# Performance work log

Measured on AMD Instinct MI355X. Metric: run time of the kernel, lower is better.

Reference implementation:

```python
import jax, jax.numpy as jnp
import numpy as np

B_SZ, SEQ, D_MODEL, D_INNER, D_STATE, D_CONV = 2, 2048, 768, 1536, 16, 4
EPS = 1e-6


def setup_inputs() -> dict:
    key = jax.random.key(0)
    ks = jax.random.split(key, 8)
    sc = lambda n: 1.0 / np.sqrt(n)
    x = jax.random.normal(ks[0], (B_SZ, SEQ, D_MODEL), jnp.float32)
    norm_w = jnp.ones((D_MODEL,), jnp.float32)
    w_in = jax.random.normal(ks[1], (D_MODEL, 2 * D_INNER), jnp.float32) * sc(D_MODEL)
    conv_w = jax.random.normal(ks[2], (D_INNER, D_CONV), jnp.float32) * sc(D_CONV)
    conv_b = jnp.zeros((D_INNER,), jnp.float32)
    w_x = jax.random.normal(ks[3], (D_INNER, 2 * D_STATE + 1), jnp.float32) * sc(D_INNER)
    w_dt = jax.random.normal(ks[4], (D_INNER,), jnp.float32)
    b_dt = jnp.zeros((D_INNER,), jnp.float32)
    A_log = jnp.log(jnp.broadcast_to(jnp.arange(1, D_STATE + 1, dtype=jnp.float32), (D_INNER, D_STATE)))
    D = jnp.ones((D_INNER,), jnp.float32)
    w_out = jax.random.normal(ks[5], (D_INNER, D_MODEL), jnp.float32) * sc(D_INNER)
    return dict(x=x, norm_w=norm_w, w_in=w_in, conv_w=conv_w, conv_b=conv_b,
                w_x=w_x, w_dt=w_dt, b_dt=b_dt, A_log=A_log, D=D, w_out=w_out)


def _rmsnorm(x, w):
    xf = x.astype(jnp.float32)
    rms = jax.lax.rsqrt(jnp.mean(xf * xf, axis=-1, keepdims=True) + EPS)
    return (xf * rms).astype(x.dtype) * w


def _silu(x):
    return x * jax.nn.sigmoid(x)


def _s6_forward(x, norm_w, w_in, conv_w, conv_b, w_x, w_dt, b_dt, A_log, D, w_out):
    Bsz, S, Dm = x.shape
    Di, K = conv_w.shape
    Ds = A_log.shape[1]
    residual = x
    xn = _rmsnorm(x, norm_w)
    xz = xn @ w_in                                 # (B,S,2*Di)
    x_main, z = jnp.split(xz, 2, axis=-1)
    # causal depthwise conv1d: pad left K-1, keep first S outputs
    lhs = x_main.transpose(0, 2, 1)                # (B,Di,S)
    rhs = conv_w[:, None, :]                       # (Di,1,K)
    conv = jax.lax.conv_general_dilated(
        lhs, rhs, window_strides=(1,), padding=[(K - 1, 0)],
        dimension_numbers=('NCH', 'OIH', 'NCH'), feature_group_count=Di)
    x_main = (conv + conv_b[None, :, None]).transpose(0, 2, 1)  # (B,S,Di)
    x_main = _silu(x_main)
    x_ssm = x_main @ w_x                           # (B,S,2*Ds+1)
    Bp = x_ssm[..., :Ds]                           # (B,S,Ds)
    Cp = x_ssm[..., Ds:2 * Ds]                     # (B,S,Ds)
    dt_raw = x_ssm[..., -1:]                       # (B,S,1)
    dt = jax.nn.softplus(dt_raw * w_dt[None, None, :] + b_dt)  # (B,S,Di)
    A = -jnp.exp(A_log)                            # (Di,Ds)

    def step(h, inp):
        xt, dtt, Bt, Ct = inp                      # (B,Di),(B,Di),(B,Ds),(B,Ds)
        dA = jnp.exp(A[None] * dtt[..., None])     # (B,Di,Ds)
        h = dA * h + (dtt * xt)[..., None] * Bt[:, None, :]
        y = jnp.einsum('bds,bs->bd', h, Ct)
        return h, y

    h0 = jnp.zeros((Bsz, Di, Ds), x_main.dtype)
    xs = (x_main.transpose(1, 0, 2), dt.transpose(1, 0, 2),
          Bp.transpose(1, 0, 2), Cp.transpose(1, 0, 2))
    _, ys = jax.lax.scan(step, h0, xs)             # ys: (S,B,Di)
    y = ys.transpose(1, 0, 2)
    y = y + x_main * D
    y = y * _silu(z)
    return residual + y @ w_out                    # dropout is identity at eval


def reference(x, norm_w, w_in, conv_w, conv_b, w_x, w_dt, b_dt, A_log, D, w_out):
    return _s6_forward(x, norm_w, w_in, conv_w, conv_b, w_x, w_dt, b_dt, A_log, D, w_out)
```

## Files before the change

### kernel.cpp

```cpp
#include <hip/hip_runtime.h>
#include <math.h>


#define DM   768
#define DI   1536
#define DS2  16
#define SEQN 2048
#define BSZ  2
#define NROWS (BSZ*SEQN)
#define CHUNK 32
#define NCHUNK (SEQN/CHUNK)

#define AS1 __attribute__((address_space(1)))
#define AS3 __attribute__((address_space(3)))

typedef short short8 __attribute__((ext_vector_type(8)));
typedef short short4v __attribute__((ext_vector_type(4)));
typedef float f32x4 __attribute__((ext_vector_type(4)));

__device__ __forceinline__ unsigned short f2bf(float f) {
  unsigned u = __builtin_bit_cast(unsigned, f);
  unsigned r = (u + 0x7FFFu + ((u >> 16) & 1u)) >> 16;
  return (unsigned short)r;
}
__device__ __forceinline__ float bf2f(short s) {
  unsigned u = ((unsigned)(unsigned short)s) << 16;
  return __builtin_bit_cast(float, u);
}

template<int N> __device__ __forceinline__ void waitcnt_vm() {
  if constexpr (N == 0)      asm volatile("s_waitcnt vmcnt(0)" ::: "memory");
  else if constexpr (N == 2) asm volatile("s_waitcnt vmcnt(2)" ::: "memory");
  else if constexpr (N == 3) asm volatile("s_waitcnt vmcnt(3)" ::: "memory");
  else if constexpr (N == 4) asm volatile("s_waitcnt vmcnt(4)" ::: "memory");
  else if constexpr (N == 6) asm volatile("s_waitcnt vmcnt(6)" ::: "memory");
}

__device__ __forceinline__ void transpose_body(const float* __restrict__ src,
                                               int rows, int cols,
                                               short* __restrict__ dst,
                                               int bx, int by, int tid) {
  __shared__ float t[32][33];
  int r0 = by * 32, c0 = bx * 32;
  int lr = tid >> 3, lc4 = (tid & 7) * 4;
  float4 v = *reinterpret_cast<const float4*>(&src[(size_t)(r0 + lr) * cols + c0 + lc4]);
  t[lr][lc4 + 0] = v.x; t[lr][lc4 + 1] = v.y; t[lr][lc4 + 2] = v.z; t[lr][lc4 + 3] = v.w;
  __syncthreads();
  int orow = tid >> 3, oc4 = (tid & 7) * 4;
  short4v o;
  o.x = (short)f2bf(t[oc4 + 0][orow]); o.y = (short)f2bf(t[oc4 + 1][orow]);
  o.z = (short)f2bf(t[oc4 + 2][orow]); o.w = (short)f2bf(t[oc4 + 3][orow]);
  *reinterpret_cast<short4v*>(&dst[(size_t)(c0 + orow) * rows + r0 + oc4]) = o;
}

__global__ __launch_bounds__(256) void prep_k(
    const float* __restrict__ x, const float* __restrict__ nw,
    short* __restrict__ xn,
    const float* __restrict__ w_in, short* __restrict__ winT,
    const float* __restrict__ w_out, short* __restrict__ woutT,
    const float* __restrict__ wx, short* __restrict__ wxT48) {
  const int bid = blockIdx.x;
  const int tid = threadIdx.x;
  if (bid < 1024) {
    int wv = tid >> 6, lane = tid & 63;
    int row = bid * 4 + wv;
    const float* xr = x + (size_t)row * DM;
    float4 v[3];
    float s = 0.f;
#pragma unroll
    for (int i = 0; i < 3; ++i) {
      v[i] = *reinterpret_cast<const float4*>(&xr[(i * 64 + lane) * 4]);
      s = fmaf(v[i].x, v[i].x, s); s = fmaf(v[i].y, v[i].y, s);
      s = fmaf(v[i].z, v[i].z, s); s = fmaf(v[i].w, v[i].w, s);
    }
#pragma unroll
    for (int off = 32; off >= 1; off >>= 1) s += __shfl_xor(s, off, 64);
    float rs = rsqrtf(s * (1.f / DM) + 1e-6f);
#pragma unroll
    for (int i = 0; i < 3; ++i) {
      const float4 w = *reinterpret_cast<const float4*>(&nw[(i * 64 + lane) * 4]);
      short4v o;
      o.x = (short)f2bf(v[i].x * rs * w.x); o.y = (short)f2bf(v[i].y * rs * w.y);
      o.z = (short)f2bf(v[i].z * rs * w.z); o.w = (short)f2bf(v[i].w * rs * w.w);
      *reinterpret_cast<short4v*>(&xn[(size_t)row * DM + (i * 64 + lane) * 4]) = o;
    }
  } else if (bid < 1024 + 2304) {
    int i2 = bid - 1024;
    transpose_body(w_in, DM, 2 * DI, winT, i2 % 96, i2 / 96, tid);
  } else if (bid < 1024 + 2304 + 1152) {
    int i3 = bid - (1024 + 2304);
    transpose_body(w_out, DI, DM, woutT, i3 % 24, i3 / 24, tid);
  } else {
    int idx = (bid - (1024 + 2304 + 1152)) * 256 + tid;
    if (idx < DI * 33) {
      int k = idx / 33, j = idx % 33;
      wxT48[(size_t)j * DI + k] = (short)f2bf(wx[idx]);
    }
  }
}

template<int BM, int BN, bool OUTBF>
__global__ __launch_bounds__(512) void gemm_bf16(
    const short* __restrict__ A, int lda,
    const short* __restrict__ Bt, int ldb,
    void* __restrict__ Cv, int ldc, int K,
    const float* __restrict__ res, int ldr)
{
  constexpr int WM = BM / 2, WN = BN / 4;
  constexpr int MI = WM / 16, NJ = WN / 16;
  constexpr int ACH = BM / 8, BCH = BN / 8;
  constexpr int CPW = (ACH + BCH) / 8;
  static_assert((ACH + BCH) % 8 == 0, "chunks must split across 8 waves");
  __shared__ __align__(16) short As[2 * BM * 64];
  __shared__ __align__(16) short Bs[2 * BN * 64];
  const int tid = threadIdx.x;
  const int w = tid >> 6, lane = tid & 63;
  const int wr = w >> 2, wc = w & 3;
  const int m0 = blockIdx.y * BM, n0 = blockIdx.x * BN;
  const int l15 = lane & 15, l4 = lane >> 4;
  const int srow = lane >> 3;
  const int ksw = (((lane & 7) ^ srow) * 8);
  const int rx = l15 & 7;

  f32x4 acc[MI][NJ];
#pragma unroll
  for (int i = 0; i < MI; ++i)
#pragma unroll
    for (int j = 0; j < NJ; ++j) acc[i][j] = (f32x4){0.f, 0.f, 0.f, 0.f};

  auto STAGE = [&](int buf, int k0) {
#pragma unroll
    for (int q = 0; q < CPW; ++q) {
      int c = w * CPW + q;
      if (c < ACH) {
        __builtin_amdgcn_global_load_lds(
            (const AS1 unsigned int*)(A + (size_t)(m0 + 8 * c + srow) * lda + k0 + ksw),
            (AS3 unsigned int*)((char*)As + buf * (BM * 128) + c * 1024), 16, 0, 0);
      } else {
        int c2 = c - ACH;
        __builtin_amdgcn_global_load_lds(
            (const AS1 unsigned int*)(Bt + (size_t)(n0 + 8 * c2 + srow) * ldb + k0 + ksw),
            (AS3 unsigned int*)((char*)Bs + buf * (BN * 128) + c2 * 1024), 16, 0, 0);
      }
    }
  };

  STAGE(0, 0);
  int cur = 0;
  const int NT = K / 64;
  for (int t = 0; t < NT; ++t) {
    __builtin_amdgcn_sched_barrier(0);
    __builtin_amdgcn_s_barrier();
    if (t + 1 < NT) {
      STAGE(cur ^ 1, (t + 1) * 64);
      waitcnt_vm<CPW>();
    } else {
      waitcnt_vm<0>();
    }
    __builtin_amdgcn_sched_barrier(0);
    __builtin_amdgcn_s_barrier();
    __builtin_amdgcn_sched_barrier(0);
    const short* Ab = As + cur * BM * 64;
    const short* Bb = Bs + cur * BN * 64;
    __builtin_amdgcn_s_setprio(1);
#pragma unroll
    for (int kk = 0; kk < 2; ++kk) {
      short8 a[MI], b[NJ];
#pragma unroll
      for (int i = 0; i < MI; ++i)
        a[i] = *reinterpret_cast<const short8*>(
            &Ab[(wr * WM + i * 16 + l15) * 64 + (((kk * 4 + l4) ^ rx) * 8)]);
#pragma unroll
      for (int j = 0; j < NJ; ++j)
        b[j] = *reinterpret_cast<const short8*>(
            &Bb[(wc * WN + j * 16 + l15) * 64 + (((kk * 4 + l4) ^ rx) * 8)]);
#pragma unroll
      for (int i = 0; i < MI; ++i)
#pragma unroll
        for (int j = 0; j < NJ; ++j)
          acc[i][j] = __builtin_amdgcn_mfma_f32_16x16x32_bf16(a[i], b[j], acc[i][j], 0, 0, 0);
    }
    __builtin_amdgcn_s_setprio(0);
    cur ^= 1;
  }

#pragma unroll
  for (int i = 0; i < MI; ++i) {
#pragma unroll
    for (int j = 0; j < NJ; ++j) {
      int col = n0 + wc * WN + j * 16 + l15;
#pragma unroll
      for (int r = 0; r < 4; ++r) {
        int row = m0 + wr * WM + i * 16 + l4 * 4 + r;
        float v = acc[i][j][r];
        if constexpr (OUTBF) {
          ((short*)Cv)[(size_t)row * ldc + col] = (short)f2bf(v);
        } else {
          if (res) v += res[(size_t)row * ldr + col];
          ((float*)Cv)[(size_t)row * ldc + col] = v;
        }
      }
    }
  }
}

__global__ __launch_bounds__(256) void conv_silu_k(const short* __restrict__ xz,
                                                   const float* __restrict__ cw,
                                                   const float* __restrict__ cb,
                                                   short* __restrict__ xc) {
  int idx = blockIdx.x * 256 + threadIdx.x;
  int d8 = (idx % (DI / 8)) * 8;
  int bt = idx / (DI / 8);
  int t = bt & (SEQN - 1);
  short8 rb[4];
#pragma unroll
  for (int rr = 0; rr < 4; ++rr) {
    int trow = t - 3 + rr;
    rb[rr] = (trow >= 0)
        ? *reinterpret_cast<const short8*>(&xz[(size_t)(bt - 3 + rr) * 3072 + d8])
        : (short8){0, 0, 0, 0, 0, 0, 0, 0};
  }
  const float4 ba = *reinterpret_cast<const float4*>(&cb[d8]);
  const float4 bbq = *reinterpret_cast<const float4*>(&cb[d8 + 4]);
  const float bias[8] = {ba.x, ba.y, ba.z, ba.w, bbq.x, bbq.y, bbq.z, bbq.w};
  short8 o;
#pragma unroll
  for (int i = 0; i < 8; ++i) {
    const float4 cwv = *reinterpret_cast<const float4*>(&cw[(size_t)(d8 + i) * 4]);
    float acc = bias[i];
    acc = fmaf(bf2f(rb[0][i]), cwv.x, acc);
    acc = fmaf(bf2f(rb[1][i]), cwv.y, acc);
    acc = fmaf(bf2f(rb[2][i]), cwv.z, acc);
    acc = fmaf(bf2f(rb[3][i]), cwv.w, acc);
    o[i] = (short)f2bf(acc / (1.f + __expf(-acc)));
  }
  *reinterpret_cast<short8*>(&xc[(size_t)bt * DI + d8]) = o;
}

__global__ __launch_bounds__(512) void xssm_gemm_k(
    const short* __restrict__ xc, const short* __restrict__ wxT48,
    float* __restrict__ xout)
{
  __shared__ float red[8][16][48];
  const int tid = threadIdx.x;
  const int wv = tid >> 6, lane = tid & 63;
  const int l15 = lane & 15, l4 = lane >> 4;
  const int m0 = blockIdx.x * 16;
  const int kbase = wv * 192 + l4 * 8;

  f32x4 acc[3];
#pragma unroll
  for (int j = 0; j < 3; ++j) acc[j] = (f32x4){0.f, 0.f, 0.f, 0.f};

  const short* arow = xc + (size_t)(m0 + l15) * DI + kbase;
#pragma unroll
  for (int ks = 0; ks < 6; ++ks) {
    short8 a = *reinterpret_cast<const short8*>(arow + ks * 32);
#pragma unroll
    for (int j = 0; j < 3; ++j) {
      short8 b = *reinterpret_cast<const short8*>(
          &wxT48[(size_t)(j * 16 + l15) * DI + kbase + ks * 32]);
      acc[j] = __builtin_amdgcn_mfma_f32_16x16x32_bf16(a, b, acc[j], 0, 0, 0);
    }
  }
#pragma unroll
  for (int j = 0; j < 3; ++j)
#pragma unroll
    for (int r = 0; r < 4; ++r)
      red[wv][l4 * 4 + r][j * 16 + l15] = acc[j][r];
  __syncthreads();
  for (int i = tid; i < 16 * 48; i += 512) {
    int row = i / 48, col = i % 48;
    float s = 0.f;
#pragma unroll
    for (int v = 0; v < 8; ++v) s += red[v][row][col];
    xout[(size_t)(m0 + row) * 48 + col] = s;
  }
}

__global__ __launch_bounds__(256) void scan_part1(
    const short* __restrict__ xc,
    const float* __restrict__ xout,
    const float* __restrict__ w_dt, const float* __restrict__ b_dt,
    const float* __restrict__ A_log,
    float* __restrict__ hL, float* __restrict__ Tsum)
{
  const int blk = blockIdx.x;
  const int c  = blk % NCHUNK;
  const int db = (blk / NCHUNK) % (DI / 256);
  const int b  = blk / (NCHUNK * (DI / 256));
  const int tid = threadIdx.x;
  const int d = db * 256 + tid;
  const size_t cb = (size_t)b * SEQN + c * CHUNK;

  __shared__ float sB[CHUNK][16];
  __shared__ float sdt[CHUNK];
  if (tid < CHUNK * 4) {
    int row = tid >> 2, q = tid & 3;
    *reinterpret_cast<float4*>(&sB[row][q * 4]) =
        *reinterpret_cast<const float4*>(&xout[(cb + row) * 48 + q * 4]);
  }
  if (tid < CHUNK) sdt[tid] = xout[(cb + tid) * 48 + 32];
  __syncthreads();

  const float wdt = w_dt[d], bdt = b_dt[d];
  float a[DS2], h[DS2];
#pragma unroll
  for (int q = 0; q < 4; ++q) {
    float4 al = *reinterpret_cast<const float4*>(&A_log[(size_t)d * DS2 + q * 4]);
    a[q * 4 + 0] = -__expf(al.x); a[q * 4 + 1] = -__expf(al.y);
    a[q * 4 + 2] = -__expf(al.z); a[q * 4 + 3] = -__expf(al.w);
  }
#pragma unroll
  for (int n = 0; n < DS2; ++n) h[n] = 0.f;
  float T = 0.f;

#pragma unroll 2
  for (int tt = 0; tt < CHUNK; ++tt) {
    float v = fmaf(sdt[tt], wdt, bdt);
    float dtv = (v > 15.f) ? v : __logf(1.f + __expf(v));
    T += dtv;
    float xv = bf2f(xc[(cb + tt) * DI + d]);
    float s = dtv * xv;
    float bb[DS2];
#pragma unroll
    for (int q = 0; q < 4; ++q)
      *reinterpret_cast<float4*>(&bb[q * 4]) =
          *reinterpret_cast<const float4*>(&sB[tt][q * 4]);
#pragma unroll
    for (int n = 0; n < DS2; ++n)
      h[n] = fmaf(__expf(a[n] * dtv), h[n], s * bb[n]);
  }

  const size_t base = (size_t)(b * NCHUNK + c) * DI + d;
#pragma unroll
  for (int q = 0; q < 4; ++q)
    *reinterpret_cast<float4*>(&hL[base * 16 + q * 4]) =
        *reinterpret_cast<const float4*>(&h[q * 4]);
  Tsum[base] = T;
}

__global__ __launch_bounds__(256) void scan_combine_k(
    float* __restrict__ hLH, const float* __restrict__ Tsum,
    const float* __restrict__ A_log)
{
  int g = blockIdx.x * 256 + threadIdx.x;
  int n = g & 15;
  int d = (g >> 4) % DI;
  int b = g / (DI * DS2);
  const float a = -__expf(A_log[(size_t)d * DS2 + n]);
  float h = 0.f;
  for (int c = 0; c < NCHUNK; ++c) {
    size_t base = (size_t)(b * NCHUNK + c) * DI + d;
    float hl = hLH[base * 16 + n];
    float T = Tsum[base];
    float hprev = h;
    h = fmaf(__expf(a * T), h, hl);
    hLH[base * 16 + n] = hprev;
  }
}

__global__ __launch_bounds__(256) void scan_part3(
    const short* __restrict__ xc,
    const short* __restrict__ xz,
    short* __restrict__ ybf,
    const float* __restrict__ xout,
    const float* __restrict__ w_dt, const float* __restrict__ b_dt,
    const float* __restrict__ A_log, const float* __restrict__ Dp,
    const float* __restrict__ Hinit)
{
  const int blk = blockIdx.x;
  const int c  = blk % NCHUNK;
  const int db = (blk / NCHUNK) % (DI / 256);
  const int b  = blk / (NCHUNK * (DI / 256));
  const int tid = threadIdx.x;
  const int d = db * 256 + tid;
  const size_t cb = (size_t)b * SEQN + c * CHUNK;

  __shared__ float sB[CHUNK][16], sC[CHUNK][16];
  __shared__ float sdt[CHUNK];
  if (tid < CHUNK * 4) {
    int row = tid >> 2, q = tid & 3;
    *reinterpret_cast<float4*>(&sB[row][q * 4]) =
        *reinterpret_cast<const float4*>(&xout[(cb + row) * 48 + q * 4]);
  } else if (tid < CHUNK * 8) {
    int i = tid - CHUNK * 4;
    int row = i >> 2, q = i & 3;
    *reinterpret_cast<float4*>(&sC[row][q * 4]) =
        *reinterpret_cast<const float4*>(&xout[(cb + row) * 48 + 16 + q * 4]);
  }
  if (tid < CHUNK) sdt[tid] = xout[(cb + tid) * 48 + 32];

  const float wdt = w_dt[d], bdt = b_dt[d];
  const float Dd = Dp[d];
  float a[DS2], h[DS2];
#pragma unroll
  for (int q = 0; q < 4; ++q) {
    float4 al = *reinterpret_cast<const float4*>(&A_log[(size_t)d * DS2 + q * 4]);
    a[q * 4 + 0] = -__expf(al.x); a[q * 4 + 1] = -__expf(al.y);
    a[q * 4 + 2] = -__expf(al.z); a[q * 4 + 3] = -__expf(al.w);
  }
  const size_t base = (size_t)(b * NCHUNK + c) * DI + d;
#pragma unroll
  for (int q = 0; q < 4; ++q)
    *reinterpret_cast<float4*>(&h[q * 4]) =
        *reinterpret_cast<const float4*>(&Hinit[base * 16 + q * 4]);
  __syncthreads();

#pragma unroll 2
  for (int tt = 0; tt < CHUNK; ++tt) {
    float v = fmaf(sdt[tt], wdt, bdt);
    float dtv = (v > 15.f) ? v : __logf(1.f + __expf(v));
    float xv = bf2f(xc[(cb + tt) * DI + d]);
    float s = dtv * xv;
    float bb[DS2], cc[DS2];
#pragma unroll
    for (int q = 0; q < 4; ++q) {
      *reinterpret_cast<float4*>(&bb[q * 4]) =
          *reinterpret_cast<const float4*>(&sB[tt][q * 4]);
      *reinterpret_cast<float4*>(&cc[q * 4]) =
          *reinterpret_cast<const float4*>(&sC[tt][q * 4]);
    }
    float y = 0.f;
#pragma unroll
    for (int n = 0; n < DS2; ++n) {
      h[n] = fmaf(__expf(a[n] * dtv), h[n], s * bb[n]);
      y = fmaf(h[n], cc[n], y);
    }
    const size_t rr = cb + tt;
    float z = bf2f(xz[rr * 3072 + DI + d]);
    float yo = fmaf(xv, Dd, y);
    ybf[rr * DI + d] = (short)f2bf(yo * (z / (1.f + __expf(-z))));
  }
}

extern "C" void kernel_launch(void* const* d_in, const int* in_sizes, int n_in,
                              void* d_out, int out_size, void* d_ws, size_t ws_size,
                              hipStream_t stream) {
  const float* x      = (const float*)d_in[0];
  const float* norm_w = (const float*)d_in[1];
  const float* w_in   = (const float*)d_in[2];
  const float* conv_w = (const float*)d_in[3];
  const float* conv_b = (const float*)d_in[4];
  const float* w_x    = (const float*)d_in[5];
  const float* w_dt   = (const float*)d_in[6];
  const float* b_dt   = (const float*)d_in[7];
  const float* A_log  = (const float*)d_in[8];
  const float* Dp     = (const float*)d_in[9];
  const float* w_out  = (const float*)d_in[10];
  float* out = (float*)d_out;

  float* ws   = (float*)d_ws;
  float* xout = ws;
  float* hL   = xout + (size_t)NROWS * 48;
  float* Tsum = hL + (size_t)BSZ * NCHUNK * DI * 16;
  short* wxT48= (short*)(Tsum + (size_t)BSZ * NCHUNK * DI);
  short* xzb  = wxT48 + (size_t)48 * DI;
  short* xcb  = xzb + (size_t)NROWS * 2 * DI;
  short* xnb  = xcb + (size_t)NROWS * DI;
  short* winT = xnb + (size_t)NROWS * DM;
  short* woutT= winT + (size_t)2 * DI * DM;
  short* ybf  = woutT + (size_t)DM * DI;

  prep_k<<<1024 + 2304 + 1152 + 198, 256, 0, stream>>>(
      x, norm_w, xnb, w_in, winT, w_out, woutT, w_x, wxT48);

  gemm_bf16<128, 128, true><<<dim3(2 * DI / 128, NROWS / 128), 512, 0, stream>>>(
      xnb, DM, winT, DM, xzb, 2 * DI, DM, nullptr, 0);

  conv_silu_k<<<(NROWS * DI / 8) / 256, 256, 0, stream>>>(xzb, conv_w, conv_b, xcb);
  xssm_gemm_k<<<NROWS / 16, 512, 0, stream>>>(xcb, wxT48, xout);

  const int nblk = BSZ * (DI / 256) * NCHUNK;
  scan_part1<<<nblk, 256, 0, stream>>>(xcb, xout, w_dt, b_dt, A_log, hL, Tsum);
  scan_combine_k<<<(BSZ * DI * DS2) / 256, 256, 0, stream>>>(hL, Tsum, A_log);
  scan_part3<<<nblk, 256, 0, stream>>>(xcb, xzb, ybf, xout, w_dt, b_dt,
                                       A_log, Dp, hL);

  gemm_bf16<128, 64, false><<<dim3(DM / 64, NROWS / 128), 512, 0, stream>>>(
      ybf, DI, woutT, DI, out, DM, DI, x, DM);
}
```

Before: 154.6 us.

## Fuse conv+SiLU into x-projection GEMM and remap GEMM blocks for XCD locality

Merges the causal depthwise conv + SiLU kernel into the small x_ssm projection GEMM. Each block computes its 16 rows of conv output into LDS and still writes them to global memory for the scan kernels. This removes one launch and the global re-read of xc. The bf16 GEMM gains a configurable wave grid, with the output GEMM switched to a 4x2 wave layout, and a block-id remap that groups consecutive tiles onto the same XCD (chiplet) for L2 reuse. The fused kernel uses about 49KB of LDS per block, which may lower occupancy.

```diff
diff --git a/kernel.cpp b/kernel.cpp
--- a/kernel.cpp
+++ b/kernel.cpp
@@ -30,10 +30,8 @@
 
 template<int N> __device__ __forceinline__ void waitcnt_vm() {
   if constexpr (N == 0)      asm volatile("s_waitcnt vmcnt(0)" ::: "memory");
-  else if constexpr (N == 2) asm volatile("s_waitcnt vmcnt(2)" ::: "memory");
   else if constexpr (N == 3) asm volatile("s_waitcnt vmcnt(3)" ::: "memory");
   else if constexpr (N == 4) asm volatile("s_waitcnt vmcnt(4)" ::: "memory");
-  else if constexpr (N == 6) asm volatile("s_waitcnt vmcnt(6)" ::: "memory");
 }
 
 __device__ __forceinline__ void transpose_body(const float* __restrict__ src,
@@ -99,24 +97,29 @@
   }
 }
 
-template<int BM, int BN, bool OUTBF>
+template<int BM, int BN, int WGM, int WGN, bool OUTBF>
 __global__ __launch_bounds__(512) void gemm_bf16(
     const short* __restrict__ A, int lda,
     const short* __restrict__ Bt, int ldb,
     void* __restrict__ Cv, int ldc, int K,
     const float* __restrict__ res, int ldr)
 {
-  constexpr int WM = BM / 2, WN = BN / 4;
+  constexpr int WM = BM / WGM, WN = BN / WGN;
   constexpr int MI = WM / 16, NJ = WN / 16;
   constexpr int ACH = BM / 8, BCH = BN / 8;
   constexpr int CPW = (ACH + BCH) / 8;
-  static_assert((ACH + BCH) % 8 == 0, "chunks must split across 8 waves");
+  static_assert(WGM * WGN == 8 && (ACH + BCH) % 8 == 0, "wave/chunk split");
   __shared__ __align__(16) short As[2 * BM * 64];
   __shared__ __align__(16) short Bs[2 * BN * 64];
   const int tid = threadIdx.x;
   const int w = tid >> 6, lane = tid & 63;
-  const int wr = w >> 2, wc = w & 3;
-  const int m0 = blockIdx.y * BM, n0 = blockIdx.x * BN;
+  const int wr = w / WGN, wc = w % WGN;
+
+  const int nwg = gridDim.x * gridDim.y;
+  const int lid = blockIdx.y * gridDim.x + blockIdx.x;
+  const int orig = (lid & 7) * (nwg >> 3) + (lid >> 3);
+  const int m0 = (orig / gridDim.x) * BM, n0 = (orig % gridDim.x) * BN;
+
   const int l15 = lane & 15, l4 = lane >> 4;
   const int srow = lane >> 3;
   const int ksw = (((lane & 7) ^ srow) * 8);
@@ -204,58 +207,62 @@
   }
 }
 
-__global__ __launch_bounds__(256) void conv_silu_k(const short* __restrict__ xz,
-                                                   const float* __restrict__ cw,
-                                                   const float* __restrict__ cb,
-                                                   short* __restrict__ xc) {
-  int idx = blockIdx.x * 256 + threadIdx.x;
-  int d8 = (idx % (DI / 8)) * 8;
-  int bt = idx / (DI / 8);
-  int t = bt & (SEQN - 1);
-  short8 rb[4];
-#pragma unroll
-  for (int rr = 0; rr < 4; ++rr) {
-    int trow = t - 3 + rr;
-    rb[rr] = (trow >= 0)
-        ? *reinterpret_cast<const short8*>(&xz[(size_t)(bt - 3 + rr) * 3072 + d8])
-        : (short8){0, 0, 0, 0, 0, 0, 0, 0};
-  }
-  const float4 ba = *reinterpret_cast<const float4*>(&cb[d8]);
-  const float4 bbq = *reinterpret_cast<const float4*>(&cb[d8 + 4]);
-  const float bias[8] = {ba.x, ba.y, ba.z, ba.w, bbq.x, bbq.y, bbq.z, bbq.w};
-  short8 o;
-#pragma unroll
-  for (int i = 0; i < 8; ++i) {
-    const float4 cwv = *reinterpret_cast<const float4*>(&cw[(size_t)(d8 + i) * 4]);
-    float acc = bias[i];
-    acc = fmaf(bf2f(rb[0][i]), cwv.x, acc);
-    acc = fmaf(bf2f(rb[1][i]), cwv.y, acc);
-    acc = fmaf(bf2f(rb[2][i]), cwv.z, acc);
-    acc = fmaf(bf2f(rb[3][i]), cwv.w, acc);
-    o[i] = (short)f2bf(acc / (1.f + __expf(-acc)));
-  }
-  *reinterpret_cast<short8*>(&xc[(size_t)bt * DI + d8]) = o;
-}
-
-__global__ __launch_bounds__(512) void xssm_gemm_k(
-    const short* __restrict__ xc, const short* __restrict__ wxT48,
-    float* __restrict__ xout)
+__global__ __launch_bounds__(512) void xssm_fused_k(
+    const short* __restrict__ xz,
+    const float* __restrict__ cw, const float* __restrict__ cb,
+    const short* __restrict__ wxT48,
+    short* __restrict__ xc, float* __restrict__ xout)
 {
+  constexpr int LP = 1544;
+  __shared__ __align__(16) short xs[16 * LP];
   __shared__ float red[8][16][48];
   const int tid = threadIdx.x;
+  const int m0 = blockIdx.x * 16;
+
+#pragma unroll
+  for (int i = 0; i < 6; ++i) {
+    const int task = i * 512 + tid;
+    const int row = task / 192;
+    const int g8 = (task % 192) * 8;
+    const int bt = m0 + row;
+    const int t = bt & (SEQN - 1);
+    short8 rb[4];
+#pragma unroll
+    for (int rr = 0; rr < 4; ++rr) {
+      int trow = t - 3 + rr;
+      rb[rr] = (trow >= 0)
+          ? *reinterpret_cast<const short8*>(&xz[(size_t)(bt - 3 + rr) * 3072 + g8])
+          : (short8){0, 0, 0, 0, 0, 0, 0, 0};
+    }
+    const float4 ba = *reinterpret_cast<const float4*>(&cb[g8]);
+    const float4 bbq = *reinterpret_cast<const float4*>(&cb[g8 + 4]);
+    const float bias[8] = {ba.x, ba.y, ba.z, ba.w, bbq.x, bbq.y, bbq.z, bbq.w};
+    short8 o;
+#pragma unroll
+    for (int ii = 0; ii < 8; ++ii) {
+      const float4 cwv = *reinterpret_cast<const float4*>(&cw[(size_t)(g8 + ii) * 4]);
+      float acc = bias[ii];
+      acc = fmaf(bf2f(rb[0][ii]), cwv.x, acc);
+      acc = fmaf(bf2f(rb[1][ii]), cwv.y, acc);
+      acc = fmaf(bf2f(rb[2][ii]), cwv.z, acc);
+      acc = fmaf(bf2f(rb[3][ii]), cwv.w, acc);
+      o[ii] = (short)f2bf(acc / (1.f + __expf(-acc)));
+    }
+    *reinterpret_cast<short8*>(&xc[(size_t)bt * DI + g8]) = o;
+    *reinterpret_cast<short8*>(&xs[row * LP + g8]) = o;
+  }
+  __syncthreads();
+
   const int wv = tid >> 6, lane = tid & 63;
   const int l15 = lane & 15, l4 = lane >> 4;
-  const int m0 = blockIdx.x * 16;
   const int kbase = wv * 192 + l4 * 8;
 
   f32x4 acc[3];
 #pragma unroll
   for (int j = 0; j < 3; ++j) acc[j] = (f32x4){0.f, 0.f, 0.f, 0.f};
-
-  const short* arow = xc + (size_t)(m0 + l15) * DI + kbase;
 #pragma unroll
   for (int ks = 0; ks < 6; ++ks) {
-    short8 a = *reinterpret_cast<const short8*>(arow + ks * 32);
+    short8 a = *reinterpret_cast<const short8*>(&xs[l15 * LP + kbase + ks * 32]);
 #pragma unroll
     for (int j = 0; j < 3; ++j) {
       short8 b = *reinterpret_cast<const short8*>(
@@ -465,11 +472,11 @@
   prep_k<<<1024 + 2304 + 1152 + 198, 256, 0, stream>>>(
       x, norm_w, xnb, w_in, winT, w_out, woutT, w_x, wxT48);
 
-  gemm_bf16<128, 128, true><<<dim3(2 * DI / 128, NROWS / 128), 512, 0, stream>>>(
+  gemm_bf16<128, 128, 2, 4, true><<<dim3(2 * DI / 128, NROWS / 128), 512, 0, stream>>>(
       xnb, DM, winT, DM, xzb, 2 * DI, DM, nullptr, 0);
 
-  conv_silu_k<<<(NROWS * DI / 8) / 256, 256, 0, stream>>>(xzb, conv_w, conv_b, xcb);
-  xssm_gemm_k<<<NROWS / 16, 512, 0, stream>>>(xcb, wxT48, xout);
+  xssm_fused_k<<<NROWS / 16, 512, 0, stream>>>(xzb, conv_w, conv_b, wxT48,
+                                               xcb, xout);
 
   const int nblk = BSZ * (DI / 256) * NCHUNK;
   scan_part1<<<nblk, 256, 0, stream>>>(xcb, xout, w_dt, b_dt, A_log, hL, Tsum);
@@ -477,6 +484,6 @@
   scan_part3<<<nblk, 256, 0, stream>>>(xcb, xzb, ybf, xout, w_dt, b_dt,
                                        A_log, Dp, hL);
 
-  gemm_bf16<128, 64, false><<<dim3(DM / 64, NROWS / 128), 512, 0, stream>>>(
+  gemm_bf16<128, 64, 4, 2, false><<<dim3(DM / 64, NROWS / 128), 512, 0, stream>>>(
       ybf, DI, woutT, DI, out, DM, DI, x, DM);
 }
```

Result: slower. 157.8 us (+2.1%).
